# Performance work log

Hardware: AMD Instinct MI355X
Metric: run time of the kernel (lower is better)

Reference implementation:

```python
import math
import jax, jax.numpy as jnp
import numpy as np

MODEL_DIM = 2048
NUM_EXPERTS = 64
NUM_TOKENS = 8192
CAPACITY_FACTOR = 1.0


def setup_inputs() -> dict:
    key = jax.random.key(0)
    kx, kw = jax.random.split(key)
    x = jax.random.normal(kx, (NUM_TOKENS, MODEL_DIM), dtype=jnp.float32)
    # Linear(model_dim, num_experts, bias=False): weight [E, D], y = x @ W.T
    wg = jax.random.normal(kw, (NUM_EXPERTS, MODEL_DIM), dtype=jnp.float32) * (1.0 / math.sqrt(MODEL_DIM))
    return {"x": x, "wg": wg}


def reference(x, wg):
    # ---- gate projection: logits [S, E] ----
    logits = jnp.einsum('sd,ed->se', x, wg)
    gates = jax.nn.softmax(logits, axis=1)
    S, E = gates.shape
    # training mode -> capacity = capacity_factor * ceil(S / E)  (static)
    capacity = int(CAPACITY_FACTOR * math.ceil(S / E))

    # ---- top-1 expert selection ----
    indices1_s = jnp.argmax(gates, axis=1)                      # [S]
    mask1 = jax.nn.one_hot(indices1_s, E, dtype=jnp.int32)      # [S, E]

    # gate value of the chosen expert per token
    gates1_s = jnp.sum(gates * mask1.astype(gates.dtype), axis=1)  # [S]

    # position of each token within its expert's queue (cumsum over tokens)
    locations1 = jnp.cumsum(mask1, axis=0) - 1                  # [S, E]

    # ---- load-balancing auxiliary loss ----
    me = jnp.mean(gates, axis=0)                                # [E]
    ce = jnp.mean(mask1.astype(gates.dtype), axis=0)            # [E]
    l_aux = jnp.mean(me * ce) * (E * E)

    # ---- capacity enforcement: drop tokens beyond expert capacity ----
    mask1 = mask1 * (locations1 < capacity).astype(mask1.dtype) # [S, E]
    locations1_s = jnp.sum(locations1 * mask1, axis=1)          # [S]

    # ---- combine / dispatch tensors ----
    gates1 = gates1_s[:, None] * mask1.astype(gates.dtype)      # [S, E]
    locations1_sc = jax.nn.one_hot(locations1_s, capacity, dtype=gates.dtype)  # [S, C]
    # torch.bmm(gates1[:, :, None], locations1_sc[:, None, :]) == outer product per token
    combine1_sec = jnp.einsum('se,sc->sec', gates1, locations1_sc)  # [S, E, C]
    dispatch_mask = combine1_sec > 0                            # bool [S, E, C]

    return l_aux, combine1_sec, dispatch_mask
```

## Files before the change

### kernel.cpp

```cpp
#include <hip/hip_runtime.h>
#include <math.h>

#define DIM     2048
#define NEXP    64
#define CAP     128
#define NTOK    8192
#define NTILE   256
#define KC      256
#define NCH     (DIM/KC)
#define XWSTR   260
#define PSTR    68
#define RF      67108864
#define RF4     16777216
#define FBLK    2048
#define FCH     16384

typedef float vfloat4 __attribute__((ext_vector_type(4)));

__global__ __launch_bounds__(512, 2) void gate(
    const float* __restrict__ x, const float* __restrict__ wg,
    int* __restrict__ expert_idx, float* __restrict__ gate_top,
    int* __restrict__ rank,
    float* __restrict__ me_partial, int* __restrict__ counts)
{
    __shared__ __align__(16) float smem[(32 + NEXP) * XWSTR];
    __shared__ float me_w[8 * NEXP];
    __shared__ int   cnt_w[8 * NEXP];
    __shared__ int   exp_s[32];

    float* xs = smem;
    float* ws = smem + 32 * XWSTR;

    const int tid  = threadIdx.x;
    const int gb   = blockIdx.x;
    const int tok0 = gb * 32;
    const int sl   = tid >> 5;
    const int i    = tid & 31;
    const int tg   = i & 3;
    const int eg   = i >> 2;
    const int kb   = sl * 16;

    float acc[8][8] = {};

    for (int ch = 0; ch < NCH; ++ch) {
        const int k0 = ch * KC;
        #pragma unroll
        for (int q = 0; q < 4; ++q) {
            int id = tid + (q << 9);
            int r = id >> 6, c = id & 63;
            float4 v = *(const float4*)(x + (size_t)(tok0 + r) * DIM + k0 + 4 * c);
            *(float4*)(&xs[r * XWSTR + 4 * c]) = v;
        }
        #pragma unroll
        for (int q = 0; q < 8; ++q) {
            int id = tid + (q << 9);
            int r = id >> 6, c = id & 63;
            float4 v = *(const float4*)(wg + (size_t)r * DIM + k0 + 4 * c);
            *(float4*)(&ws[r * XWSTR + 4 * c]) = v;
        }
        __syncthreads();

        #pragma unroll
        for (int q2 = 0; q2 < 4; ++q2) {
            const int kk = kb + 4 * q2;
            float4 xt[8], we[8];
            #pragma unroll
            for (int j = 0; j < 8; ++j)
                xt[j] = *(const float4*)(&xs[(tg + 4 * j) * XWSTR + kk]);
            #pragma unroll
            for (int m = 0; m < 8; ++m)
                we[m] = *(const float4*)(&ws[(eg + 8 * m) * XWSTR + kk]);
            #pragma unroll
            for (int j = 0; j < 8; ++j)
                #pragma unroll
                for (int m = 0; m < 8; ++m) {
                    acc[j][m] = fmaf(xt[j].x, we[m].x, acc[j][m]);
                    acc[j][m] = fmaf(xt[j].y, we[m].y, acc[j][m]);
                    acc[j][m] = fmaf(xt[j].z, we[m].z, acc[j][m]);
                    acc[j][m] = fmaf(xt[j].w, we[m].w, acc[j][m]);
                }
        }
        __syncthreads();
    }

    float* part = smem;
    float* lgt  = smem + 8 * 32 * PSTR;
    if (sl >= 8) {
        #pragma unroll
        for (int j = 0; j < 8; ++j)
            #pragma unroll
            for (int m = 0; m < 8; ++m)
                part[((sl - 8) * 32 + tg + 4 * j) * PSTR + eg + 8 * m] = acc[j][m];
    }
    __syncthreads();
    if (sl < 8) {
        #pragma unroll
        for (int j = 0; j < 8; ++j)
            #pragma unroll
            for (int m = 0; m < 8; ++m) {
                int idx = (sl * 32 + tg + 4 * j) * PSTR + eg + 8 * m;
                part[idx] += acc[j][m];
            }
    }
    __syncthreads();

    {
        int t  = tid >> 4;
        int e0 = (tid & 15) << 2;
        float4 a = {0, 0, 0, 0};
        #pragma unroll
        for (int s2 = 0; s2 < 8; ++s2) {
            float4 p = *(const float4*)(&part[(s2 * 32 + t) * PSTR + e0]);
            a.x += p.x; a.y += p.y; a.z += p.z; a.w += p.w;
        }
        *(float4*)(&lgt[t * PSTR + e0]) = a;
    }
    __syncthreads();

    const int lane = tid & 63;
    const int wv   = tid >> 6;
    float me_acc  = 0.0f;
    int   cnt_acc = 0;
    #pragma unroll
    for (int r4 = 0; r4 < 4; ++r4) {
        int row = wv * 4 + r4;
        float v = lgt[row * PSTR + lane];
        float m = v; int mi = lane;
        #pragma unroll
        for (int off = 32; off > 0; off >>= 1) {
            float om  = __shfl_xor(m, off);
            int   omi = __shfl_xor(mi, off);
            if (om > m || (om == m && omi < mi)) { m = om; mi = omi; }
        }
        float ex = __expf(v - m);
        float sm = ex;
        #pragma unroll
        for (int off = 32; off > 0; off >>= 1) sm += __shfl_xor(sm, off);
        me_acc += ex / sm;
        if (lane == mi) {
            expert_idx[tok0 + row] = mi;
            gate_top[tok0 + row]   = 1.0f / sm;
            exp_s[row] = mi;
            ++cnt_acc;
        }
    }
    me_w[wv * NEXP + lane]  = me_acc;
    cnt_w[wv * NEXP + lane] = cnt_acc;
    __syncthreads();

    if (tid < 32) {
        int e = exp_s[tid];
        int rk = 0;
        for (int u = 0; u < tid; ++u) rk += (exp_s[u] == e) ? 1 : 0;
        rank[tok0 + tid] = rk;
    }
    if (tid < NEXP) {
        float ms = 0.f; int cs = 0;
        #pragma unroll
        for (int w = 0; w < 8; ++w) { ms += me_w[w * NEXP + tid]; cs += cnt_w[w * NEXP + tid]; }
        me_partial[gb * NEXP + tid] = ms;
        counts[gb * NEXP + tid]     = cs;
    }
}

__global__ __launch_bounds__(1024) void prefix_pos(
    const float* __restrict__ me_partial, const int* __restrict__ counts,
    const int* __restrict__ expert_idx, const int* __restrict__ rank,
    int* __restrict__ pos_g, float* __restrict__ laux)
{
    __shared__ int   bo_l[NTILE * NEXP];
    __shared__ int   cnt_l[16 * NEXP];
    __shared__ float me_l[16 * NEXP];
    __shared__ int   cnt_tot[NEXP];
    __shared__ float me_tot[NEXP];

    const int tid = threadIdx.x;
    const int e   = tid & 63;
    const int g   = tid >> 6;

    int cs = 0; float ms = 0.f;
    #pragma unroll
    for (int i = 0; i < 16; ++i) {
        int t = g * 16 + i;
        cs += counts[t * NEXP + e];
        ms += me_partial[t * NEXP + e];
    }
    cnt_l[g * NEXP + e] = cs;
    me_l[g * NEXP + e]  = ms;
    __syncthreads();

    if (g == 0) {
        int run = 0; float mt = 0.f;
        #pragma unroll
        for (int i = 0; i < 16; ++i) {
            int c = cnt_l[i * NEXP + e];
            cnt_l[i * NEXP + e] = run;
            run += c;
            mt  += me_l[i * NEXP + e];
        }
        cnt_tot[e] = run;
        me_tot[e]  = mt;
    }
    __syncthreads();

    int run = cnt_l[g * NEXP + e];
    #pragma unroll
    for (int i = 0; i < 16; ++i) {
        int t = g * 16 + i;
        bo_l[t * NEXP + e] = run;
        run += counts[t * NEXP + e];
    }
    __syncthreads();

    if (tid < NEXP) {
        float v = (me_tot[e] / (float)NTOK) * ((float)cnt_tot[e] / (float)NTOK);
        #pragma unroll
        for (int off = 32; off > 0; off >>= 1) v += __shfl_xor(v, off);
        if (e == 0) laux[0] = v * (float)NEXP;
    }

    #pragma unroll
    for (int ii = 0; ii < 8; ++ii) {
        int s  = tid + (ii << 10);
        int ex = expert_idx[s];
        int loc = bo_l[(s >> 5) * NEXP + ex] + rank[s];
        pos_g[s] = (loc < CAP) ? (1 + s * (NEXP * CAP) + ex * CAP + loc) : -1;
    }
}

__global__ __launch_bounds__(512) void fill_patch(
    const int* __restrict__ pos_g, const float* __restrict__ gate_top,
    const float* __restrict__ laux, float* __restrict__ out)
{
    const int tid = threadIdx.x;
    const int b   = blockIdx.x;
    vfloat4* o4 = reinterpret_cast<vfloat4*>(out);
    const vfloat4 z4 = {0.f, 0.f, 0.f, 0.f};

    const size_t base = (size_t)b * FCH + tid;
    #pragma unroll
    for (int k = 0; k < 32; ++k)
        __builtin_nontemporal_store(z4, &o4[base + (size_t)(k << 9)]);
    if (b == FBLK - 1 && tid == 511)
        out[134217728ull] = 0.0f;
    __syncthreads();

    if (tid < 18) {
        const int isD = tid >= 9;
        const int r   = tid - 9 * isD;
        const int sb  = isD ? (b - 1024) : b;
        const int s   = 8 * sb - 1 + r;
        if (s >= 0 && s < NTOK) {
            const int p = pos_g[s];
            if (p >= 0) {
                const int gi = p + (isD ? RF : 0);
                const int F  = gi >> 2;
                const int lo = b * FCH;
                const int hi = lo + FCH + ((b == FBLK - 1) ? 1 : 0);
                if (F >= lo && F < hi)
                    out[(size_t)gi] = isD ? 1.0f : gate_top[s];
            }
        }
    }
    if (b == 0 && tid == 18) out[0] = laux[0];
}

extern "C" void kernel_launch(void* const* d_in, const int* in_sizes, int n_in,
                              void* d_out, int out_size, void* d_ws, size_t ws_size,
                              hipStream_t stream)
{
    const float* x  = (const float*)d_in[0];
    const float* wg = (const float*)d_in[1];
    float* out = (float*)d_out;

    char* ws = (char*)d_ws;
    int*   expert_idx = (int*)  (ws);
    float* gate_top   = (float*)(ws + 32768);
    int*   rank       = (int*)  (ws + 65536);
    float* me_partial = (float*)(ws + 98304);
    int*   counts     = (int*)  (ws + 163840);
    int*   pos_g      = (int*)  (ws + 229376);
    float* laux       = (float*)(ws + 262144);

    gate<<<NTILE, 512, 0, stream>>>(x, wg, expert_idx, gate_top, rank,
                                    me_partial, counts);
    prefix_pos<<<1, 1024, 0, stream>>>(me_partial, counts, expert_idx, rank,
                                       pos_g, laux);
    fill_patch<<<FBLK, 512, 0, stream>>>(pos_g, gate_top, laux, out);
}
```

Baseline: 607.5 us.

## Split zero-fill from patch kernel and run fill before gating

Replaces the fused fill_patch kernel with a separate zero-fill kernel launched first, plus a small scatter kernel that writes only the non-zero combine and dispatch entries at the end. The fill now uses regular stores instead of nontemporal stores, and smaller blocks that each cover half as much. This removes the per-block range checks and makes the scatter trivial. The same stream still serializes the kernels, and dropping nontemporal stores may raise cache pollution on the roughly half-gigabyte output.

```diff
diff --git a/kernel.cpp b/kernel.cpp
--- a/kernel.cpp
+++ b/kernel.cpp
@@ -11,11 +11,22 @@
 #define XWSTR   260
 #define PSTR    68
 #define RF      67108864
-#define RF4     16777216
-#define FBLK    2048
-#define FCH     16384
+#define FBLK    4096
+#define FCH     8192
 
 typedef float vfloat4 __attribute__((ext_vector_type(4)));
+
+__global__ __launch_bounds__(256) void fill(float* __restrict__ out)
+{
+    vfloat4* o4 = reinterpret_cast<vfloat4*>(out);
+    const vfloat4 z4 = {0.f, 0.f, 0.f, 0.f};
+    const size_t base = (size_t)blockIdx.x * FCH + threadIdx.x;
+    #pragma unroll
+    for (int k = 0; k < 32; ++k)
+        o4[base + (size_t)(k << 8)] = z4;
+    if (blockIdx.x == 0 && threadIdx.x == 0)
+        out[134217728ull] = 0.0f;
+}
 
 __global__ __launch_bounds__(512, 2) void gate(
     const float* __restrict__ x, const float* __restrict__ wg,
@@ -228,41 +239,17 @@
     }
 }
 
-__global__ __launch_bounds__(512) void fill_patch(
+__global__ __launch_bounds__(64) void patch(
     const int* __restrict__ pos_g, const float* __restrict__ gate_top,
     const float* __restrict__ laux, float* __restrict__ out)
 {
-    const int tid = threadIdx.x;
-    const int b   = blockIdx.x;
-    vfloat4* o4 = reinterpret_cast<vfloat4*>(out);
-    const vfloat4 z4 = {0.f, 0.f, 0.f, 0.f};
-
-    const size_t base = (size_t)b * FCH + tid;
-    #pragma unroll
-    for (int k = 0; k < 32; ++k)
-        __builtin_nontemporal_store(z4, &o4[base + (size_t)(k << 9)]);
-    if (b == FBLK - 1 && tid == 511)
-        out[134217728ull] = 0.0f;
-    __syncthreads();
-
-    if (tid < 18) {
-        const int isD = tid >= 9;
-        const int r   = tid - 9 * isD;
-        const int sb  = isD ? (b - 1024) : b;
-        const int s   = 8 * sb - 1 + r;
-        if (s >= 0 && s < NTOK) {
-            const int p = pos_g[s];
-            if (p >= 0) {
-                const int gi = p + (isD ? RF : 0);
-                const int F  = gi >> 2;
-                const int lo = b * FCH;
-                const int hi = lo + FCH + ((b == FBLK - 1) ? 1 : 0);
-                if (F >= lo && F < hi)
-                    out[(size_t)gi] = isD ? 1.0f : gate_top[s];
-            }
-        }
-    }
-    if (b == 0 && tid == 18) out[0] = laux[0];
+    const int s = blockIdx.x * 64 + threadIdx.x;
+    const int p = pos_g[s];
+    if (p >= 0) {
+        out[(size_t)p]      = gate_top[s];
+        out[(size_t)p + RF] = 1.0f;
+    }
+    if (s == 0) out[0] = laux[0];
 }
 
 extern "C" void kernel_launch(void* const* d_in, const int* in_sizes, int n_in,
@@ -282,9 +269,10 @@
     int*   pos_g      = (int*)  (ws + 229376);
     float* laux       = (float*)(ws + 262144);
 
+    fill<<<FBLK, 256, 0, stream>>>(out);
     gate<<<NTILE, 512, 0, stream>>>(x, wg, expert_idx, gate_top, rank,
                                     me_partial, counts);
     prefix_pos<<<1, 1024, 0, stream>>>(me_partial, counts, expert_idx, rank,
                                        pos_g, laux);
-    fill_patch<<<FBLK, 512, 0, stream>>>(pos_g, gate_top, laux, out);
-}
+    patch<<<128, 64, 0, stream>>>(pos_g, gate_top, laux, out);
+}
```

New measurement: 612.3 us. About the same (+0.8%).
